# Performance work log

Measured on AMD Instinct MI355X. Metric: run time of the kernel, lower is better.

## Reference

```python
import jax, jax.numpy as jnp
import numpy as np

B, N, E, D = 32, 144, 127, 512   # batch, seq (forced to 144 by additive PE), embed_size, encoding_size
H, DK, DV = 8, 64, 64            # heads, dim_k, dim_v
F = 32 * D                       # forward_expansion=32 (default)
L = 4                            # num_layers
EPS = 1e-5


def setup_inputs() -> dict:
    key = jax.random.key(0)
    ks = jax.random.split(key, 20)
    s = 0.02
    x = jax.random.normal(ks[0], (B, N, E), jnp.float32)
    # causal mask: True = masked (future positions)
    future_mask = jnp.broadcast_to(jnp.triu(jnp.ones((N, N), bool), k=1), (B, N, N))
    inp = {
        'batch_size': B,
        'x': x,
        'future_mask': future_mask,
        'Wenc': jax.random.normal(ks[1], (E + 1, D), jnp.float32) * s,
        'benc': jnp.zeros((D,), jnp.float32),
        'Wq': jax.random.normal(ks[2], (L, D, H * DK), jnp.float32) * s,
        'Wk': jax.random.normal(ks[3], (L, D, H * DK), jnp.float32) * s,
        'Wv': jax.random.normal(ks[4], (L, D, H * DV), jnp.float32) * s,
        'Wo': jax.random.normal(ks[5], (L, H * DV, D), jnp.float32) * s,
        'bo': jnp.zeros((L, D), jnp.float32),
        'ln1_g': jnp.ones((L, D), jnp.float32), 'ln1_b': jnp.zeros((L, D), jnp.float32),
        'ln2_g': jnp.ones((L, D), jnp.float32), 'ln2_b': jnp.zeros((L, D), jnp.float32),
        'ln3_g': jnp.ones((L, D), jnp.float32), 'ln3_b': jnp.zeros((L, D), jnp.float32),
        'W1': jax.random.normal(ks[6], (L, D, F), jnp.float32) * s,
        'b1': jnp.zeros((L, F), jnp.float32),
        'W2': jax.random.normal(ks[7], (L, F, D), jnp.float32) * s,
        'b2': jnp.zeros((L, D), jnp.float32),
        'Wdec': jax.random.normal(ks[8], (D, E), jnp.float32) * s,
        'bdec': jnp.zeros((E,), jnp.float32),
    }
    return inp


def _layernorm(x, g, b):
    mu = jnp.mean(x, axis=-1, keepdims=True)
    var = jnp.var(x, axis=-1, keepdims=True)
    return (x - mu) * jax.lax.rsqrt(var + EPS) * g + b


def _mha(values_in, keys_in, query_in, mask, Wq, Wk, Wv, Wo, bo):
    b = query_in.shape[0]
    q = (query_in @ Wq).reshape(b, -1, H, DK).transpose(0, 2, 1, 3)   # [b,H,N,DK]
    k = (keys_in @ Wk).reshape(b, -1, H, DK).transpose(0, 2, 1, 3)
    v = (values_in @ Wv).reshape(b, -1, H, DV).transpose(0, 2, 1, 3)  # [b,H,N,DV]
    scores = jnp.einsum('bhnk,bhmk->bhnm', q, k)  # NOTE: no 1/sqrt(dk) scaling in original
    if mask is not None:
        scores = jnp.where(mask[:, None, :, :], jnp.float32(-1e20), scores)
    attn = jax.nn.softmax(scores, axis=-1)
    # torch.einsum('bhnn,bhnv->bhnv') takes the DIAGONAL of attn and scales v elementwise
    diag = jnp.diagonal(attn, axis1=2, axis2=3)  # [b,H,N]
    out = diag[..., None] * v                    # [b,H,N,DV]
    out = out.transpose(0, 2, 1, 3).reshape(b, -1, H * DV)
    return out @ Wo + bo


def reference(batch_size, x, future_mask, Wenc, benc, Wq, Wk, Wv, Wo, bo,
              ln1_g, ln1_b, ln2_g, ln2_b, ln3_g, ln3_b, W1, b1, W2, b2, Wdec, bdec):
    # Additive positional encoding: append arange(N)/max as extra channel
    pe = (jnp.arange(N, dtype=jnp.float32) / jnp.float32(N - 1))[None, :, None]
    xp = jnp.concatenate([x, jnp.broadcast_to(pe, (x.shape[0], N, 1))], axis=2)
    xe = xp @ Wenc + benc  # [B,N,D]
    out = xe
    for l in range(L):
        a = _mha(out, out, out, future_mask, Wq[l], Wk[l], Wv[l], Wo[l], bo[l])
        q = _layernorm(a + xe, ln1_g[l], ln1_b[l])
        a = _mha(xe, xe, q, None, Wq[l], Wk[l], Wv[l], Wo[l], bo[l])
        ff = jax.nn.relu(a @ W1[l] + b1[l]) @ W2[l] + b2[l]
        ao = _layernorm(ff + a, ln2_g[l], ln2_b[l])
        ff2 = jax.nn.relu(ao @ W1[l] + b1[l]) @ W2[l] + b2[l]
        out = _layernorm(ao + ff2, ln3_g[l], ln3_b[l])
    return out @ Wdec + bdec  # [B,N,E]
```

## Files before the change

### kernel.cpp

```cpp
#include <hip/hip_runtime.h>
#include <stdint.h>


typedef unsigned short u16;
typedef unsigned int   u32;
typedef __attribute__((ext_vector_type(8))) short s16x8;
typedef __attribute__((ext_vector_type(4))) float f32x4;

#define AS1 __attribute__((address_space(1)))
#define AS3 __attribute__((address_space(3)))

__device__ __forceinline__ float bf2f(u16 h) { return __uint_as_float(((u32)h) << 16); }
__device__ __forceinline__ u16 f2bf(float f) {
  u32 u = __float_as_uint(f);
  u32 r = (u + 0x7fffu + ((u >> 16) & 1u)) >> 16;
  return (u16)r;
}
__device__ __forceinline__ void gl_lds16(const u16* g, u16* l) {
  __builtin_amdgcn_global_load_lds((const AS1 void*)g, (AS3 void*)l, 16, 0, 0);
}

template<bool BIAS, bool RELU, bool OBF>
__global__ __launch_bounds__(256, 2)
void gemm_bt(const u16* __restrict__ A, int lda,
             const u16* __restrict__ Bt, int ldb,
             void* __restrict__ Cv, int ldc,
             const float* __restrict__ bias,
             int K, int nreal, long long sstride)
{
  __shared__ __align__(16) u16 As[128 * 32];
  __shared__ __align__(16) u16 Bs[128 * 32];
  const int tid  = threadIdx.x;
  const int wave = tid >> 6, lane = tid & 63;
  const int m0 = blockIdx.x * 128, n0 = blockIdx.y * 128;
  const long long koff = (long long)blockIdx.z * K;
  A  += (size_t)m0 * lda + koff;
  Bt += (size_t)n0 * ldb + koff;

  const int ch0 = tid, ch1 = tid + 256;
  const u16* ga0 = A  + (size_t)(ch0 >> 2) * lda + (ch0 & 3) * 8;
  const u16* ga1 = A  + (size_t)(ch1 >> 2) * lda + (ch1 & 3) * 8;
  const u16* gb0 = Bt + (size_t)(ch0 >> 2) * ldb + (ch0 & 3) * 8;
  const u16* gb1 = Bt + (size_t)(ch1 >> 2) * ldb + (ch1 & 3) * 8;
  u16* la0 = &As[ch0 * 8];
  u16* la1 = &As[ch1 * 8];
  u16* lb0 = &Bs[ch0 * 8];
  u16* lb1 = &Bs[ch1 * 8];

  const int wr = (wave >> 1) * 64, wc = (wave & 1) * 64;
  const int fr = lane & 15, kq = lane >> 4;

  f32x4 acc[4][4] = {};

  for (int kt = 0; kt < K; kt += 32) {
    gl_lds16(ga0, la0); gl_lds16(ga1, la1);
    gl_lds16(gb0, lb0); gl_lds16(gb1, lb1);
    ga0 += 32; ga1 += 32; gb0 += 32; gb1 += 32;
    __syncthreads();
    s16x8 af[4], bfv[4];
#pragma unroll
    for (int i = 0; i < 4; ++i)
      af[i] = *(const s16x8*)&As[(wr + i * 16 + fr) * 32 + kq * 8];
#pragma unroll
    for (int i = 0; i < 4; ++i)
      bfv[i] = *(const s16x8*)&Bs[(wc + i * 16 + fr) * 32 + kq * 8];
#pragma unroll
    for (int i = 0; i < 4; ++i)
#pragma unroll
      for (int j = 0; j < 4; ++j)
        acc[i][j] = __builtin_amdgcn_mfma_f32_16x16x32_bf16(af[i], bfv[j], acc[i][j], 0, 0, 0);
    __syncthreads();
  }

#pragma unroll
  for (int j = 0; j < 4; ++j) {
    const int ccol = n0 + wc + j * 16 + fr;
    if (ccol >= nreal) continue;
    const float bv = BIAS ? bias[ccol] : 0.0f;
#pragma unroll
    for (int i = 0; i < 4; ++i) {
#pragma unroll
      for (int r = 0; r < 4; ++r) {
        const int crow = m0 + wr + i * 16 + kq * 4 + r;
        float v = acc[i][j][r] + bv;
        if (RELU) v = fmaxf(v, 0.0f);
        if (OBF) ((u16*)Cv)[(size_t)crow * ldc + ccol] = f2bf(v);
        else ((float*)Cv + (size_t)blockIdx.z * sstride)[(size_t)crow * ldc + ccol] = v;
      }
    }
  }
}

__global__ void tcvt(u16* __restrict__ Wt, const float* __restrict__ W,
                     int K, int N, int Npad)
{
  __shared__ float t[32][33];
  const int n0 = blockIdx.x * 32, k0 = blockIdx.y * 32;
  const int tx = threadIdx.x, ty = threadIdx.y;
#pragma unroll
  for (int i = 0; i < 4; ++i) {
    int k = k0 + ty + i * 8, n = n0 + tx;
    t[ty + i * 8][tx] = (k < K && n < N) ? W[(size_t)k * N + n] : 0.f;
  }
  __syncthreads();
#pragma unroll
  for (int i = 0; i < 4; ++i) {
    int n = n0 + ty + i * 8, k = k0 + tx;
    if (n < Npad) Wt[(size_t)n * K + k] = f2bf(t[tx][ty + i * 8]);
  }
}

template<bool CAUSAL>
__global__ __launch_bounds__(192)
void attn_diag(float* __restrict__ diag,
               const u16* __restrict__ Q, int ldq,
               const u16* __restrict__ Kp, int ldk)
{
  __shared__ float Kl[144][64];
  const int bh = blockIdx.x;
  const int b = bh >> 3, h = bh & 7;
  const int tid = threadIdx.x;

  for (int c = tid; c < 144 * 8; c += 192) {
    int m = c >> 3, c8 = c & 7;
    uint4 u = *(const uint4*)(Kp + (size_t)(b * 144 + m) * ldk + h * 64 + c8 * 8);
    float* dst = &Kl[m][c8 * 8];
    dst[0] = __uint_as_float(u.x << 16); dst[1] = __uint_as_float(u.x & 0xffff0000u);
    dst[2] = __uint_as_float(u.y << 16); dst[3] = __uint_as_float(u.y & 0xffff0000u);
    dst[4] = __uint_as_float(u.z << 16); dst[5] = __uint_as_float(u.z & 0xffff0000u);
    dst[6] = __uint_as_float(u.w << 16); dst[7] = __uint_as_float(u.w & 0xffff0000u);
  }
  __syncthreads();
  if (tid >= 144) return;
  const int n = tid;
  float q[64];
  const uint4* qp = (const uint4*)(Q + (size_t)(b * 144 + n) * ldq + h * 64);
#pragma unroll
  for (int c = 0; c < 8; ++c) {
    uint4 u = qp[c];
    q[c*8+0] = __uint_as_float(u.x << 16); q[c*8+1] = __uint_as_float(u.x & 0xffff0000u);
    q[c*8+2] = __uint_as_float(u.y << 16); q[c*8+3] = __uint_as_float(u.y & 0xffff0000u);
    q[c*8+4] = __uint_as_float(u.z << 16); q[c*8+5] = __uint_as_float(u.z & 0xffff0000u);
    q[c*8+6] = __uint_as_float(u.w << 16); q[c*8+7] = __uint_as_float(u.w & 0xffff0000u);
  }
  const int mmax = CAUSAL ? n : 143;
  float mx = -3.4e38f, sm = 0.f, sdiag = 0.f;
  for (int m = 0; m <= mmax; ++m) {
    float s0 = 0, s1 = 0, s2 = 0, s3 = 0;
#pragma unroll
    for (int c = 0; c < 64; c += 4) {
      s0 = fmaf(q[c + 0], Kl[m][c + 0], s0);
      s1 = fmaf(q[c + 1], Kl[m][c + 1], s1);
      s2 = fmaf(q[c + 2], Kl[m][c + 2], s2);
      s3 = fmaf(q[c + 3], Kl[m][c + 3], s3);
    }
    float s = (s0 + s1) + (s2 + s3);
    if (m == n) sdiag = s;
    float nmx = fmaxf(mx, s);
    sm = sm * __expf(mx - nmx) + __expf(s - nmx);
    mx = nmx;
  }
  diag[(size_t)bh * 144 + n] = __expf(sdiag - mx) / sm;
}

__global__ void scale_v(u16* __restrict__ outb, const float* __restrict__ diag,
                        const u16* __restrict__ V, int ldv)
{
  const int idx = blockIdx.x * 256 + threadIdx.x;
  const int r = idx >> 9, d = idx & 511;
  const int b = r / 144, n = r - b * 144;
  const int h = d >> 6;
  const float dg = diag[((size_t)b * 8 + h) * 144 + n];
  outb[(size_t)r * 512 + d] = f2bf(dg * bf2f(V[(size_t)r * ldv + d]));
}

__global__ __launch_bounds__(128)
void ln_dual(float* __restrict__ outf, u16* __restrict__ outb,
             const float* __restrict__ A, const float* __restrict__ Bv,
             const float* __restrict__ g, const float* __restrict__ be)
{
  const int r = blockIdx.x, t = threadIdx.x;
  float4 a = ((const float4*)(A + (size_t)r * 512))[t];
  float4 b = ((const float4*)(Bv + (size_t)r * 512))[t];
  const float x0 = a.x + b.x, x1 = a.y + b.y, x2 = a.z + b.z, x3 = a.w + b.w;
  float s = x0 + x1 + x2 + x3;
  float q = x0 * x0 + x1 * x1 + x2 * x2 + x3 * x3;
#pragma unroll
  for (int off = 32; off > 0; off >>= 1) { s += __shfl_down(s, off); q += __shfl_down(q, off); }
  __shared__ float ss[2], qs[2];
  if ((t & 63) == 0) { ss[t >> 6] = s; qs[t >> 6] = q; }
  __syncthreads();
  s = ss[0] + ss[1]; q = qs[0] + qs[1];
  const float mean = s * (1.f / 512.f);
  const float var  = q * (1.f / 512.f) - mean * mean;
  const float rs = rsqrtf(var + 1e-5f);
  float4 gg = ((const float4*)g)[t];
  float4 bb = ((const float4*)be)[t];
  const float o0 = (x0 - mean) * rs * gg.x + bb.x;
  const float o1 = (x1 - mean) * rs * gg.y + bb.y;
  const float o2 = (x2 - mean) * rs * gg.z + bb.z;
  const float o3 = (x3 - mean) * rs * gg.w + bb.w;
  if (outf) ((float4*)(outf + (size_t)r * 512))[t] = make_float4(o0, o1, o2, o3);
  if (outb) {
    uint2 u;
    u.x = (u32)f2bf(o0) | ((u32)f2bf(o1) << 16);
    u.y = (u32)f2bf(o2) | ((u32)f2bf(o3) << 16);
    ((uint2*)(outb + (size_t)r * 512))[t] = u;
  }
}

__global__ void f32_to_bf16_vec(u16* __restrict__ o, const float* __restrict__ a)
{
  const int i = blockIdx.x * 256 + threadIdx.x;
  float4 v = ((const float4*)a)[i];
  uint2 u;
  u.x = (u32)f2bf(v.x) | ((u32)f2bf(v.y) << 16);
  u.y = (u32)f2bf(v.z) | ((u32)f2bf(v.w) << 16);
  ((uint2*)o)[i] = u;
}

__global__ void reduce_ff(float* __restrict__ ff, const float* __restrict__ parts,
                          const float* __restrict__ bias)
{
  const int i = blockIdx.x * 256 + threadIdx.x;
  float4 acc = ((const float4*)bias)[i & 127];
#pragma unroll
  for (int s = 0; s < 8; ++s) {
    float4 p = ((const float4*)(parts + (size_t)s * 4608 * 512))[i];
    acc.x += p.x; acc.y += p.y; acc.z += p.z; acc.w += p.w;
  }
  ((float4*)ff)[i] = acc;
}

__global__ void build_xp(u16* __restrict__ xp, const float* __restrict__ x)
{
  const int i = blockIdx.x * 256 + threadIdx.x;
  const int r = i >> 7, e = i & 127;
  const float v = (e < 127) ? x[(size_t)r * 127 + e] : (float)(r % 144) * (1.f / 143.f);
  xp[i] = f2bf(v);
}

extern "C" void kernel_launch(void* const* d_in, const int* in_sizes, int n_in,
                              void* d_out, int out_size, void* d_ws, size_t ws_size,
                              hipStream_t stream)
{
  (void)in_sizes; (void)n_in; (void)out_size; (void)ws_size;
  const float* x    = (const float*)d_in[1];
  const float* Wenc = (const float*)d_in[3];
  const float* benc = (const float*)d_in[4];
  const float* Wq   = (const float*)d_in[5];
  const float* Wk   = (const float*)d_in[6];
  const float* Wv   = (const float*)d_in[7];
  const float* Wo   = (const float*)d_in[8];
  const float* bo   = (const float*)d_in[9];
  const float* ln1g = (const float*)d_in[10];
  const float* ln1b = (const float*)d_in[11];
  const float* ln2g = (const float*)d_in[12];
  const float* ln2b = (const float*)d_in[13];
  const float* ln3g = (const float*)d_in[14];
  const float* ln3b = (const float*)d_in[15];
  const float* W1   = (const float*)d_in[16];
  const float* b1   = (const float*)d_in[17];
  const float* W2   = (const float*)d_in[18];
  const float* b2   = (const float*)d_in[19];
  const float* Wdec = (const float*)d_in[20];
  const float* bdec = (const float*)d_in[21];

  char* w = (char*)d_ws;
  auto alloc = [&](size_t bytes) { void* p = (void*)w; w += (bytes + 255) & ~(size_t)255; return p; };
  u16*   wt_qkv = (u16*)alloc((size_t)1536 * 512 * 2);
  u16*   wt_o   = (u16*)alloc((size_t)512 * 512 * 2);
  u16*   wt_1   = (u16*)alloc((size_t)16384 * 512 * 2);
  u16*   wt_2   = (u16*)alloc((size_t)512 * 16384 * 2);
  u16*   wt_enc = (u16*)alloc((size_t)512 * 128 * 2);
  u16*   wt_dec = (u16*)alloc((size_t)128 * 512 * 2);
  float* xe_f   = (float*)alloc((size_t)4608 * 512 * 4);
  u16*   xe_bf  = (u16*)alloc((size_t)4608 * 512 * 2);
  u16*   out_bf = (u16*)alloc((size_t)4608 * 512 * 2);
  u16*   qkv_bf = (u16*)alloc((size_t)4608 * 1536 * 2);
  float* diag   = (float*)alloc((size_t)256 * 144 * 4);
  u16*   attn_bf= (u16*)alloc((size_t)4608 * 512 * 2);
  float* a1     = (float*)alloc((size_t)4608 * 512 * 4);
  u16*   qln_bf = (u16*)alloc((size_t)4608 * 512 * 2);
  float* a2     = (float*)alloc((size_t)4608 * 512 * 4);
  u16*   a2_bf  = (u16*)alloc((size_t)4608 * 512 * 2);
  u16*   hidden = (u16*)alloc((size_t)4608 * 8192 * 2);
  float* parts  = (float*)alloc((size_t)8 * 4608 * 512 * 4);
  float* ff     = (float*)alloc((size_t)4608 * 512 * 4);
  float* ao_f   = (float*)alloc((size_t)4608 * 512 * 4);
  u16*   ao_bf  = (u16*)alloc((size_t)4608 * 512 * 2);
  float* ff2    = a1;
  u16*   xp_bf  = hidden;

  const long long PSTRIDE = (long long)4608 * 512;

  tcvt<<<dim3(16, 4), dim3(32, 8), 0, stream>>>(wt_enc, Wenc, 128, 512, 512);
  tcvt<<<dim3(4, 16), dim3(32, 8), 0, stream>>>(wt_dec, Wdec, 512, 127, 128);
  build_xp<<<2304, 256, 0, stream>>>(xp_bf, x);
  gemm_bt<true, false, false><<<dim3(36, 4, 1), 256, 0, stream>>>(
      xp_bf, 128, wt_enc, 128, xe_f, 512, benc, 128, 512, 0);
  f32_to_bf16_vec<<<2304, 256, 0, stream>>>(xe_bf, xe_f);

  const u16* in_bf = xe_bf;
  for (int l = 0; l < 4; ++l) {
    const size_t wsz = (size_t)512 * 512;
    tcvt<<<dim3(16, 16), dim3(32, 8), 0, stream>>>(wt_qkv,               Wq + l * wsz, 512, 512, 512);
    tcvt<<<dim3(16, 16), dim3(32, 8), 0, stream>>>(wt_qkv + 512 * 512,   Wk + l * wsz, 512, 512, 512);
    tcvt<<<dim3(16, 16), dim3(32, 8), 0, stream>>>(wt_qkv + 1024 * 512,  Wv + l * wsz, 512, 512, 512);
    tcvt<<<dim3(16, 16), dim3(32, 8), 0, stream>>>(wt_o, Wo + l * wsz, 512, 512, 512);
    tcvt<<<dim3(512, 16), dim3(32, 8), 0, stream>>>(wt_1, W1 + (size_t)l * 512 * 16384, 512, 16384, 16384);
    tcvt<<<dim3(16, 512), dim3(32, 8), 0, stream>>>(wt_2, W2 + (size_t)l * 16384 * 512, 16384, 512, 512);

    gemm_bt<false, false, true><<<dim3(36, 12, 1), 256, 0, stream>>>(
        in_bf, 512, wt_qkv, 512, qkv_bf, 1536, nullptr, 512, 1536, 0);
    attn_diag<true><<<256, 192, 0, stream>>>(diag, qkv_bf, 1536, qkv_bf + 512, 1536);
    scale_v<<<9216, 256, 0, stream>>>(attn_bf, diag, qkv_bf + 1024, 1536);
    gemm_bt<true, false, false><<<dim3(36, 4, 1), 256, 0, stream>>>(
        attn_bf, 512, wt_o, 512, a1, 512, bo + l * 512, 512, 512, 0);
    ln_dual<<<4608, 128, 0, stream>>>(nullptr, qln_bf, a1, xe_f, ln1g + l * 512, ln1b + l * 512);

    gemm_bt<false, false, true><<<dim3(36, 4, 1), 256, 0, stream>>>(
        qln_bf, 512, wt_qkv, 512, attn_bf, 512, nullptr, 512, 512, 0);
    gemm_bt<false, false, true><<<dim3(36, 8, 1), 256, 0, stream>>>(
        xe_bf, 512, wt_qkv + 512 * 512, 512, qkv_bf, 1024, nullptr, 512, 1024, 0);
    attn_diag<false><<<256, 192, 0, stream>>>(diag, attn_bf, 512, qkv_bf, 1024);
    scale_v<<<9216, 256, 0, stream>>>(attn_bf, diag, qkv_bf + 512, 1024);
    gemm_bt<true, false, false><<<dim3(36, 4, 1), 256, 0, stream>>>(
        attn_bf, 512, wt_o, 512, a2, 512, bo + l * 512, 512, 512, 0);
    f32_to_bf16_vec<<<2304, 256, 0, stream>>>(a2_bf, a2);

    for (int c = 0; c < 2; ++c) {
      gemm_bt<true, true, true><<<dim3(36, 64, 1), 256, 0, stream>>>(
          a2_bf, 512, wt_1 + (size_t)c * 8192 * 512, 512, hidden, 8192,
          b1 + l * 16384 + c * 8192, 512, 8192, 0);
      gemm_bt<false, false, false><<<dim3(36, 4, 4), 256, 0, stream>>>(
          hidden, 8192, wt_2 + c * 8192, 16384,
          parts + (size_t)c * 4 * 4608 * 512, 512, nullptr, 2048, 512, PSTRIDE);
    }
    reduce_ff<<<2304, 256, 0, stream>>>(ff, parts, b2 + l * 512);
    ln_dual<<<4608, 128, 0, stream>>>(ao_f, ao_bf, ff, a2, ln2g + l * 512, ln2b + l * 512);

    for (int c = 0; c < 2; ++c) {
      gemm_bt<true, true, true><<<dim3(36, 64, 1), 256, 0, stream>>>(
          ao_bf, 512, wt_1 + (size_t)c * 8192 * 512, 512, hidden, 8192,
          b1 + l * 16384 + c * 8192, 512, 8192, 0);
      gemm_bt<false, false, false><<<dim3(36, 4, 4), 256, 0, stream>>>(
          hidden, 8192, wt_2 + c * 8192, 16384,
          parts + (size_t)c * 4 * 4608 * 512, 512, nullptr, 2048, 512, PSTRIDE);
    }
    reduce_ff<<<2304, 256, 0, stream>>>(ff2, parts, b2 + l * 512);
    ln_dual<<<4608, 128, 0, stream>>>(nullptr, out_bf, ao_f, ff2, ln3g + l * 512, ln3b + l * 512);
    in_bf = out_bf;
  }

  gemm_bt<true, false, false><<<dim3(36, 1, 1), 256, 0, stream>>>(
      in_bf, 512, wt_dec, 512, (float*)d_out, 127, bdec, 512, 127, 0);
}
```

Before: 3.312 ms.

## Double-buffer GEMM LDS tiles with K=64 steps and XOR-swizzled layout

Rewrites the bf16 GEMM main loop to prefetch the next K tile into a second LDS buffer while the current one feeds the MFMAs. This overlaps global loads with compute and removes one barrier per iteration. The K step grows from 32 to 64, and an XOR swizzle on LDS addresses is meant to avoid bank conflicts on fragment reads. LDS use rises to 64KB per block, which may limit occupancy under launch_bounds(256,2). The loop also assumes K is a multiple of 64.

```diff
diff --git a/kernel.cpp b/kernel.cpp
--- a/kernel.cpp
+++ b/kernel.cpp
@@ -28,8 +28,8 @@
              const float* __restrict__ bias,
              int K, int nreal, long long sstride)
 {
-  __shared__ __align__(16) u16 As[128 * 32];
-  __shared__ __align__(16) u16 Bs[128 * 32];
+  __shared__ __align__(16) u16 As[2][128 * 64];
+  __shared__ __align__(16) u16 Bs[2][128 * 64];
   const int tid  = threadIdx.x;
   const int wave = tid >> 6, lane = tid & 63;
   const int m0 = blockIdx.x * 128, n0 = blockIdx.y * 128;
@@ -37,39 +37,64 @@
   A  += (size_t)m0 * lda + koff;
   Bt += (size_t)n0 * ldb + koff;
 
-  const int ch0 = tid, ch1 = tid + 256;
-  const u16* ga0 = A  + (size_t)(ch0 >> 2) * lda + (ch0 & 3) * 8;
-  const u16* ga1 = A  + (size_t)(ch1 >> 2) * lda + (ch1 & 3) * 8;
-  const u16* gb0 = Bt + (size_t)(ch0 >> 2) * ldb + (ch0 & 3) * 8;
-  const u16* gb1 = Bt + (size_t)(ch1 >> 2) * ldb + (ch1 & 3) * 8;
-  u16* la0 = &As[ch0 * 8];
-  u16* la1 = &As[ch1 * 8];
-  u16* lb0 = &Bs[ch0 * 8];
-  u16* lb1 = &Bs[ch1 * 8];
+  const int r0 = tid >> 3;
+  const int sp = ((tid & 7) ^ (r0 & 7)) * 8;
+  const u16* gA = A  + (size_t)r0 * lda + sp;
+  const u16* gB = Bt + (size_t)r0 * ldb + sp;
+  u16* lA = &As[0][tid * 8];
+  u16* lB = &Bs[0][tid * 8];
 
   const int wr = (wave >> 1) * 64, wc = (wave & 1) * 64;
   const int fr = lane & 15, kq = lane >> 4;
+  const int s0 = ((0 * 4 + kq) ^ (fr & 7)) * 8;
+  const int s1 = ((1 * 4 + kq) ^ (fr & 7)) * 8;
 
   f32x4 acc[4][4] = {};
-
-  for (int kt = 0; kt < K; kt += 32) {
-    gl_lds16(ga0, la0); gl_lds16(ga1, la1);
-    gl_lds16(gb0, lb0); gl_lds16(gb1, lb1);
-    ga0 += 32; ga1 += 32; gb0 += 32; gb1 += 32;
+  const int NT = K >> 6;
+
+#pragma unroll
+  for (int q = 0; q < 4; ++q) gl_lds16(gA + (size_t)q * 32 * lda, lA + q * 2048);
+#pragma unroll
+  for (int q = 0; q < 4; ++q) gl_lds16(gB + (size_t)q * 32 * ldb, lB + q * 2048);
+  gA += 64; gB += 64;
+
+  for (int t = 0; t < NT; ++t) {
     __syncthreads();
-    s16x8 af[4], bfv[4];
+    const int cur = t & 1;
+    if (t + 1 < NT) {
+      u16* dA = lA + (cur ^ 1) * (128 * 64);
+      u16* dB = lB + (cur ^ 1) * (128 * 64);
+#pragma unroll
+      for (int q = 0; q < 4; ++q) gl_lds16(gA + (size_t)q * 32 * lda, dA + q * 2048);
+#pragma unroll
+      for (int q = 0; q < 4; ++q) gl_lds16(gB + (size_t)q * 32 * ldb, dB + q * 2048);
+      gA += 64; gB += 64;
+    }
+    const u16* Ab = &As[cur][0];
+    const u16* Bb = &Bs[cur][0];
+    s16x8 a0[4], a1[4], b0[4], b1[4];
+#pragma unroll
+    for (int i = 0; i < 4; ++i) {
+      const int ra = (wr + i * 16 + fr) * 64;
+      a0[i] = *(const s16x8*)&Ab[ra + s0];
+      a1[i] = *(const s16x8*)&Ab[ra + s1];
+    }
+#pragma unroll
+    for (int j = 0; j < 4; ++j) {
+      const int rb = (wc + j * 16 + fr) * 64;
+      b0[j] = *(const s16x8*)&Bb[rb + s0];
+      b1[j] = *(const s16x8*)&Bb[rb + s1];
+    }
 #pragma unroll
     for (int i = 0; i < 4; ++i)
-      af[i] = *(const s16x8*)&As[(wr + i * 16 + fr) * 32 + kq * 8];
+#pragma unroll
+      for (int j = 0; j < 4; ++j)
+        acc[i][j] = __builtin_amdgcn_mfma_f32_16x16x32_bf16(a0[i], b0[j], acc[i][j], 0, 0, 0);
 #pragma unroll
     for (int i = 0; i < 4; ++i)
-      bfv[i] = *(const s16x8*)&Bs[(wc + i * 16 + fr) * 32 + kq * 8];
-#pragma unroll
-    for (int i = 0; i < 4; ++i)
 #pragma unroll
       for (int j = 0; j < 4; ++j)
-        acc[i][j] = __builtin_amdgcn_mfma_f32_16x16x32_bf16(af[i], bfv[j], acc[i][j], 0, 0, 0);
-    __syncthreads();
+        acc[i][j] = __builtin_amdgcn_mfma_f32_16x16x32_bf16(a1[i], b1[j], acc[i][j], 0, 0, 0);
   }
 
 #pragma unroll
```

New measurement: 3.368 ms. No clear change (+1.7%).
